# Kernel optimization log

Hardware: AMD Instinct MI355X
Metric: run time of the kernel (lower is better)

Reference implementation:

```python
import jax, jax.numpy as jnp
import numpy as np

HEADS = 16
D_MODEL = 1024
D_HEAD = D_MODEL // HEADS


def setup_inputs() -> dict:
    key = jax.random.key(0)
    ks = jax.random.split(key, 9)
    s_h = 1.0 / np.sqrt(D_HEAD)
    s_m = 1.0 / np.sqrt(D_MODEL)
    return {
        "x": jax.random.normal(ks[0], (4, 2048, D_MODEL), dtype=jnp.float32),
        "Wq": jax.random.uniform(ks[1], (D_HEAD, D_HEAD), jnp.float32, -s_h, s_h),
        "bq": jax.random.uniform(ks[2], (D_HEAD,), jnp.float32, -s_h, s_h),
        "Wk": jax.random.uniform(ks[3], (D_HEAD, D_HEAD), jnp.float32, -s_h, s_h),
        "bk": jax.random.uniform(ks[4], (D_HEAD,), jnp.float32, -s_h, s_h),
        "Wv": jax.random.uniform(ks[5], (D_HEAD, D_HEAD), jnp.float32, -s_h, s_h),
        "bv": jax.random.uniform(ks[6], (D_HEAD,), jnp.float32, -s_h, s_h),
        "Wp": jax.random.uniform(ks[7], (D_MODEL, D_MODEL), jnp.float32, -s_m, s_m),
        "bp": jax.random.uniform(ks[8], (D_MODEL,), jnp.float32, -s_m, s_m),
    }


def reference(x, Wq, bq, Wk, bk, Wv, bv, Wp, bp):
    B, T, C = x.shape
    xh = x.reshape(B, T, HEADS, D_HEAD)  # [B,T,H,Dh]
    # per-head linear projections (torch Linear: x @ W.T + b)
    q = jnp.einsum('bthd,ed->bhte', xh, Wq) + bq  # [B,H,T,Dh]
    k = jnp.einsum('bthd,ed->bhte', xh, Wk) + bk
    v = jnp.einsum('bthd,ed->bhte', xh, Wv) + bv
    # NOTE: original scales by sqrt(C) = sqrt(d_model), not sqrt(d_head)
    att = jnp.einsum('bhqd,bhkd->bhqk', q, k) / jnp.sqrt(jnp.float32(C))
    att = jax.nn.softmax(att, axis=-1)
    out = jnp.einsum('bhqk,bhkd->bhqd', att, v)  # [B,H,T,Dh]
    out = out.transpose(0, 2, 1, 3).reshape(B, T, C)
    return out @ Wp.T + bp
```

## Files before the change

### kernel.cpp

```cpp
#include <hip/hip_runtime.h>
#include <hip/hip_bf16.h>
#include <cstddef>

#define B_  4
#define T_  2048
#define H_  16
#define DH  64
#define C_  1024
#define BH  64

typedef float  f32x16 __attribute__((ext_vector_type(16)));
typedef __bf16 bf16x8 __attribute__((ext_vector_type(8)));
typedef __bf16 bf16x4 __attribute__((ext_vector_type(4)));

#define MFMA32(a, b, c) __builtin_amdgcn_mfma_f32_32x32x16_bf16(a, b, c, 0, 0, 0)


__device__ __forceinline__ unsigned cvt_pk_bf16(float lo, float hi) {
    unsigned r;
    asm("v_cvt_pk_bf16_f32 %0, %1, %2" : "=v"(r) : "v"(lo), "v"(hi));
    return r;
}

__global__ __launch_bounds__(256) void wconv_kernel(
    const float* __restrict__ Wq, const float* __restrict__ Wk,
    const float* __restrict__ Wv, __bf16* __restrict__ wqkv)
{
    const int tid = blockIdx.x * 256 + threadIdx.x;
    const float* srcs[3] = {Wq, Wk, Wv};
    const int mat = tid >> 10;
    const int off = (tid & 1023) * 4;
    const float4 w4 = *(const float4*)(srcs[mat] + off);
    const unsigned lo = ((unsigned)__builtin_bit_cast(unsigned short, (__bf16)w4.y) << 16)
                      | (unsigned)__builtin_bit_cast(unsigned short, (__bf16)w4.x);
    const unsigned hi = ((unsigned)__builtin_bit_cast(unsigned short, (__bf16)w4.w) << 16)
                      | (unsigned)__builtin_bit_cast(unsigned short, (__bf16)w4.z);
    uint2 p; p.x = lo; p.y = hi;
    *(uint2*)(wqkv + mat * 4096 + off) = p;
}

__global__ __launch_bounds__(256) void qkv_kernel(
    const float* __restrict__ x,
    const __bf16* __restrict__ wqkv,
    const float* __restrict__ bq, const float* __restrict__ bk,
    const float* __restrict__ bv,
    __bf16* __restrict__ q, __bf16* __restrict__ kf, __bf16* __restrict__ vf)
{
    __shared__ __bf16 Xs[128 * 72];
    __shared__ __bf16 Ws[3][64 * 72];
    __bf16* Vtl = Xs;
    __bf16* Kst = &Ws[0][0];

    const int tt  = blockIdx.x;
    const int bh  = blockIdx.y;
    const int b   = bh >> 4, h = bh & 15;
    const int t0  = tt * 128;
    const int tid = threadIdx.x;
    const int wave = tid >> 6, lane = tid & 63;
    const int m = lane & 31, hh = lane >> 5;

    #pragma unroll
    for (int i = 0; i < 8; ++i) {
        const int idx = i * 256 + tid;
        const int r = idx >> 4, c = (idx & 15) * 4;
        const float4 x4 = *(const float4*)(x + ((size_t)(b * T_ + t0 + r)) * C_ + h * DH + c);
        const unsigned lo = ((unsigned)__builtin_bit_cast(unsigned short, (__bf16)x4.y) << 16)
                          | (unsigned)__builtin_bit_cast(unsigned short, (__bf16)x4.x);
        const unsigned hi = ((unsigned)__builtin_bit_cast(unsigned short, (__bf16)x4.w) << 16)
                          | (unsigned)__builtin_bit_cast(unsigned short, (__bf16)x4.z);
        *(unsigned*)&Xs[r * 72 + c]     = lo;
        *(unsigned*)&Xs[r * 72 + c + 2] = hi;
    }
    #pragma unroll
    for (int i = 0; i < 6; ++i) {
        const int idx = i * 256 + tid;
        const int mat_ = idx >> 9;
        const int r = (idx >> 3) & 63, c = (idx & 7) * 8;
        *(uint4*)&Ws[mat_][r * 72 + c] = *(const uint4*)(wqkv + mat_ * 4096 + r * 64 + c);
    }
    __syncthreads();

    bf16x8 xf[4];
    #pragma unroll
    for (int ks = 0; ks < 4; ++ks)
        xf[ks] = *(const bf16x8*)&Xs[(wave * 32 + m) * 72 + ks * 16 + hh * 8];
    __syncthreads();

    const float s32 = 0.03125f * 1.4426950408889634f;

    unsigned kpk[16];

    #pragma unroll
    for (int mat = 0; mat < 3; ++mat) {
        f32x16 acc0 = {}, acc1 = {};
        #pragma unroll
        for (int ks = 0; ks < 4; ++ks) {
            const bf16x8 w0 = *(const bf16x8*)&Ws[mat][(m) * 72 + ks * 16 + hh * 8];
            const bf16x8 w1 = *(const bf16x8*)&Ws[mat][(32 + m) * 72 + ks * 16 + hh * 8];
            acc0 = MFMA32(xf[ks], w0, acc0);
            acc1 = MFMA32(xf[ks], w1, acc1);
        }
        const float* bias = (mat == 0) ? bq : (mat == 1) ? bk : bv;
        const float b0 = bias[m], b1 = bias[32 + m];
        #pragma unroll
        for (int r = 0; r < 16; ++r) {
            const int R = (r & 3) + 8 * (r >> 2) + 4 * hh;
            const int tloc = wave * 32 + R;
            const float v0 = acc0[r] + b0, v1 = acc1[r] + b1;
            if (mat == 0) {
                const size_t base = ((size_t)bh * T_ + t0 + tloc) * DH;
                q[base + m]      = (__bf16)(v0 * s32);
                q[base + 32 + m] = (__bf16)(v1 * s32);
            } else if (mat == 1) {
                kpk[r] = ((unsigned)__builtin_bit_cast(unsigned short, (__bf16)v1) << 16)
                       |  (unsigned)__builtin_bit_cast(unsigned short, (__bf16)v0);
            } else {
                Vtl[(m) * 136 + tloc]      = (__bf16)v0;
                Vtl[(32 + m) * 136 + tloc] = (__bf16)v1;
            }
        }
    }
    __syncthreads();

    #pragma unroll
    for (int r = 0; r < 16; ++r) {
        const int R = (r & 3) + 8 * (r >> 2) + 4 * hh;
        const int tloc = wave * 32 + R;
        Kst[tloc * 72 + m]      = __builtin_bit_cast(__bf16, (unsigned short)(kpk[r] & 0xffff));
        Kst[tloc * 72 + 32 + m] = __builtin_bit_cast(__bf16, (unsigned short)(kpk[r] >> 16));
    }

    #pragma unroll
    for (int i = 0; i < 4; ++i) {
        const int idx = i * 256 + tid;
        const int ln = idx & 63, c_ = idx >> 6;
        const int kt64l = c_ >> 3, dh = (c_ >> 2) & 1, cN = c_ & 3;
        const __bf16* src = &Vtl[(dh * 32 + (ln & 31)) * 136 + kt64l * 64 + cN * 16 + (ln >> 5) * 8];
        __bf16* dst = vf + ((((size_t)(bh * 32 + tt * 2 + kt64l) * 2 + dh) * 4 + cN) * 64 + ln) * 8;
        *(uint4*)dst = *(const uint4*)src;
    }
    __syncthreads();

    #pragma unroll
    for (int i = 0; i < 4; ++i) {
        const int idx = i * 256 + tid;
        const int ln = idx & 63, c_ = idx >> 6;
        const int kt64l = c_ >> 3, rh = (c_ >> 2) & 1, ks = c_ & 3;
        const __bf16* src = &Kst[(kt64l * 64 + rh * 32 + (ln & 31)) * 72 + ks * 16 + (ln >> 5) * 8];
        __bf16* dst = kf + ((((size_t)(bh * 32 + tt * 2 + kt64l) * 2 + rh) * 4 + ks) * 64 + ln) * 8;
        *(uint4*)dst = *(const uint4*)src;
    }
}

__global__ __launch_bounds__(256, 4) void attn_kernel(
    const __bf16* __restrict__ q, const __bf16* __restrict__ kf,
    const __bf16* __restrict__ vf, __bf16* __restrict__ o)
{
    __shared__ __bf16 Os[128 * 72];

    const int bh  = blockIdx.x;
    const int q0  = blockIdx.y * 128;
    const int tid = threadIdx.x;
    const int wave = tid >> 6, lane = tid & 63;
    const int m = lane & 31, h = lane >> 5;

    const __bf16* qb  = q  + (size_t)bh * T_ * DH;
    const __bf16* kfb = kf + (size_t)bh * (T_ * DH);
    const __bf16* vfb = vf + (size_t)bh * (T_ * DH);

    bf16x8 qf[4];
    #pragma unroll
    for (int ks = 0; ks < 4; ++ks)
        qf[ks] = *(const bf16x8*)(qb + (size_t)(q0 + wave * 32 + m) * DH + ks * 16 + h * 8);

    f32x16 O0 = {}, O1 = {};
    float lsum = 0.f;

    for (int kt = 0; kt < 32; ++kt) {
        const __bf16* kt_k = kfb + kt * 4096;
        const __bf16* kt_v = vfb + kt * 4096;
        #pragma unroll
        for (int rh = 0; rh < 2; ++rh) {
            bf16x8 kfr[4];
            #pragma unroll
            for (int ks = 0; ks < 4; ++ks)
                kfr[ks] = *(const bf16x8*)(kt_k + rh * 2048 + ks * 512 + lane * 8);
            f32x16 S = {};
            #pragma unroll
            for (int ks = 0; ks < 4; ++ks)
                S = MFMA32(kfr[ks], qf[ks], S);

            #pragma unroll
            for (int cc = 0; cc < 2; ++cc) {
                const int rb = cc * 8;
                float e0 = __builtin_amdgcn_exp2f(S[rb + 0]);
                float e1 = __builtin_amdgcn_exp2f(S[rb + 1]);
                float e2 = __builtin_amdgcn_exp2f(S[rb + 2]);
                float e3 = __builtin_amdgcn_exp2f(S[rb + 3]);
                float e4 = __builtin_amdgcn_exp2f(S[rb + 4]);
                float e5 = __builtin_amdgcn_exp2f(S[rb + 5]);
                float e6 = __builtin_amdgcn_exp2f(S[rb + 6]);
                float e7 = __builtin_amdgcn_exp2f(S[rb + 7]);
                lsum += ((e0 + e1) + (e2 + e3)) + ((e4 + e5) + (e6 + e7));
                unsigned a0 = cvt_pk_bf16(e0, e1);
                unsigned a1 = cvt_pk_bf16(e2, e3);
                unsigned b0 = cvt_pk_bf16(e4, e5);
                unsigned b1 = cvt_pk_bf16(e6, e7);
                asm("v_permlane32_swap_b32 %0, %1" : "+v"(a0), "+v"(b0));
                asm("v_permlane32_swap_b32 %0, %1" : "+v"(a1), "+v"(b1));
                const uint4 pw = {a0, a1, b0, b1};
                const bf16x8 pb = __builtin_bit_cast(bf16x8, pw);
                const int c = rh * 2 + cc;
                const bf16x8 v0 = *(const bf16x8*)(kt_v + c * 512 + lane * 8);
                const bf16x8 v1 = *(const bf16x8*)(kt_v + 2048 + c * 512 + lane * 8);
                O0 = MFMA32(v0, pb, O0);
                O1 = MFMA32(v1, pb, O1);
            }
        }
    }

    lsum += __shfl_xor(lsum, 32);
    const float linv = 1.0f / lsum;

    #pragma unroll
    for (int g = 0; g < 4; ++g) {
        bf16x4 w0, w1;
        #pragma unroll
        for (int j = 0; j < 4; ++j) {
            w0[j] = (__bf16)(O0[4 * g + j] * linv);
            w1[j] = (__bf16)(O1[4 * g + j] * linv);
        }
        const int row = (wave * 32 + m) * 72;
        *(bf16x4*)&Os[row + 8 * g + 4 * h]      = w0;
        *(bf16x4*)&Os[row + 32 + 8 * g + 4 * h] = w1;
    }
    __syncthreads();

    __bf16* ob = o + ((size_t)bh * T_ + q0) * DH;
    #pragma unroll
    for (int i = 0; i < 4; ++i) {
        const int idx = i * 256 + tid;
        const int r = idx >> 3, c = (idx & 7) * 8;
        *(uint4*)(ob + (size_t)r * DH + c) = *(uint4*)&Os[r * 72 + c];
    }
}

__global__ __launch_bounds__(256) void wpconv_kernel(
    const float* __restrict__ Wp, __bf16* __restrict__ Wpb)
{
    const size_t idx = (size_t)(blockIdx.x * 256 + threadIdx.x) * 4;
    const float4 w4 = *(const float4*)(Wp + idx);
    const unsigned lo = ((unsigned)__builtin_bit_cast(unsigned short, (__bf16)w4.y) << 16)
                      | (unsigned)__builtin_bit_cast(unsigned short, (__bf16)w4.x);
    const unsigned hi = ((unsigned)__builtin_bit_cast(unsigned short, (__bf16)w4.w) << 16)
                      | (unsigned)__builtin_bit_cast(unsigned short, (__bf16)w4.z);
    uint2 p; p.x = lo; p.y = hi;
    *(uint2*)(Wpb + idx) = p;
}

__global__ __launch_bounds__(256, 2) void proj_kernel(
    const __bf16* __restrict__ a,
    const __bf16* __restrict__ Wpb, const float* __restrict__ bp,
    float* __restrict__ out)
{
    __shared__ __bf16 As[2][128 * 72];
    __shared__ __bf16 Bs[2][128 * 72];

    const int tb = blockIdx.x, eb = blockIdx.y;
    const int tid = threadIdx.x;
    const int wave = tid >> 6, lane = tid & 63;
    const int m = lane & 31, h = lane >> 5;
    const int tok0 = tb * 128;
    const int b = tok0 >> 11, t0 = tok0 & (T_ - 1);
    const int e0 = eb * 128;

    auto aload = [&](int cb, uint4 (&ar)[4], uint4 (&br)[4]) {
        #pragma unroll
        for (int i = 0; i < 4; ++i) {
            const int idx = i * 256 + tid;
            const int r = idx >> 3, c = (idx & 7) * 8;
            ar[i] = *(const uint4*)(a + ((size_t)(b * H_ + cb) * T_ + t0 + r) * DH + c);
            br[i] = *(const uint4*)(Wpb + (size_t)(e0 + r) * C_ + cb * 64 + c);
        }
    };
    auto astore = [&](int buf, const uint4 (&ar)[4], const uint4 (&br)[4]) {
        #pragma unroll
        for (int i = 0; i < 4; ++i) {
            const int idx = i * 256 + tid;
            const int r = idx >> 3, c = (idx & 7) * 8;
            *(uint4*)&As[buf][r * 72 + c] = ar[i];
            *(uint4*)&Bs[buf][r * 72 + c] = br[i];
        }
    };

    f32x16 acc[4] = {f32x16{}, f32x16{}, f32x16{}, f32x16{}};
    uint4 areg[4], breg[4];

    aload(0, areg, breg);
    astore(0, areg, breg);

    int cur = 0;
    for (int cb = 0; cb < 16; ++cb) {
        __syncthreads();
        if (cb < 15) aload(cb + 1, areg, breg);

        #pragma unroll
        for (int ks = 0; ks < 4; ++ks) {
            const bf16x8 af = *(const bf16x8*)&As[cur][(wave * 32 + m) * 72 + ks * 16 + h * 8];
            #pragma unroll
            for (int n = 0; n < 4; ++n) {
                const bf16x8 bf = *(const bf16x8*)&Bs[cur][(n * 32 + m) * 72 + ks * 16 + h * 8];
                acc[n] = MFMA32(af, bf, acc[n]);
            }
        }

        if (cb < 15) astore(cur ^ 1, areg, breg);
        cur ^= 1;
    }

    #pragma unroll
    for (int n = 0; n < 4; ++n) {
        const int e = e0 + n * 32 + m;
        const float bias = bp[e];
        #pragma unroll
        for (int r = 0; r < 16; ++r) {
            const int R = (r & 3) + 8 * (r >> 2) + 4 * h;
            out[(size_t)(tok0 + wave * 32 + R) * C_ + e] = acc[n][r] + bias;
        }
    }
}

extern "C" void kernel_launch(void* const* d_in, const int* in_sizes, int n_in,
                              void* d_out, int out_size, void* d_ws, size_t ws_size,
                              hipStream_t stream)
{
    const float* x  = (const float*)d_in[0];
    const float* Wq = (const float*)d_in[1];
    const float* bq = (const float*)d_in[2];
    const float* Wk = (const float*)d_in[3];
    const float* bk = (const float*)d_in[4];
    const float* Wv = (const float*)d_in[5];
    const float* bv = (const float*)d_in[6];
    const float* Wp = (const float*)d_in[7];
    const float* bp = (const float*)d_in[8];

    const size_t N = (size_t)BH * T_ * DH;
    __bf16* qws  = (__bf16*)d_ws;
    __bf16* kws  = qws + N;
    __bf16* vtws = kws + N;
    __bf16* ows  = vtws + N;
    __bf16* wqkv = ows;
    __bf16* wpb  = qws;

    wconv_kernel<<<dim3(12), 256, 0, stream>>>(Wq, Wk, Wv, wqkv);
    qkv_kernel<<<dim3(16, 64), 256, 0, stream>>>(
        x, wqkv, bq, bk, bv, qws, kws, vtws);
    attn_kernel<<<dim3(64, 16), 256, 0, stream>>>(qws, kws, vtws, ows);
    wpconv_kernel<<<dim3(1024), 256, 0, stream>>>(Wp, wpb);
    proj_kernel<<<dim3(64, 8), 256, 0, stream>>>(ows, wpb, bp, (float*)d_out);
}
```

Measured before the change: 259.8 us.

## Store attention output and Wp in MFMA fragment order, drop LDS from proj

The attention kernel now writes its output in a pre-swizzled MFMA fragment layout, and the Wp conversion kernel emits bf16 weights in the same fragment order. This lets the projection GEMM load operands straight from global memory into registers with coalesced 16-byte loads, removing the LDS double buffering and barriers. The trade-off is that every block re-reads Wp fragments from global or L2 with no shared-memory reuse, and software prefetching is lost, so latency hiding depends on occupancy.

```diff
diff --git a/kernel.cpp b/kernel.cpp
--- a/kernel.cpp
+++ b/kernel.cpp
@@ -154,7 +154,7 @@
 
 __global__ __launch_bounds__(256, 4) void attn_kernel(
     const __bf16* __restrict__ q, const __bf16* __restrict__ kf,
-    const __bf16* __restrict__ vf, __bf16* __restrict__ o)
+    const __bf16* __restrict__ vf, __bf16* __restrict__ af)
 {
     __shared__ __bf16 Os[128 * 72];
 
@@ -236,86 +236,81 @@
     }
     __syncthreads();
 
-    __bf16* ob = o + ((size_t)bh * T_ + q0) * DH;
+    __bf16* ab = af + ((size_t)(bh * 16 + (q0 >> 7))) * 8192;
     #pragma unroll
     for (int i = 0; i < 4; ++i) {
         const int idx = i * 256 + tid;
-        const int r = idx >> 3, c = (idx & 7) * 8;
-        *(uint4*)(ob + (size_t)r * DH + c) = *(uint4*)&Os[r * 72 + c];
+        const int ln = idx & 63, c_ = idx >> 6;
+        const int wv = c_ >> 2, ks = c_ & 3;
+        const __bf16* src = &Os[(wv * 32 + (ln & 31)) * 72 + ks * 16 + (ln >> 5) * 8];
+        *(uint4*)(ab + c_ * 512 + ln * 8) = *(const uint4*)src;
     }
 }
 
 __global__ __launch_bounds__(256) void wpconv_kernel(
-    const float* __restrict__ Wp, __bf16* __restrict__ Wpb)
-{
-    const size_t idx = (size_t)(blockIdx.x * 256 + threadIdx.x) * 4;
-    const float4 w4 = *(const float4*)(Wp + idx);
-    const unsigned lo = ((unsigned)__builtin_bit_cast(unsigned short, (__bf16)w4.y) << 16)
-                      | (unsigned)__builtin_bit_cast(unsigned short, (__bf16)w4.x);
-    const unsigned hi = ((unsigned)__builtin_bit_cast(unsigned short, (__bf16)w4.w) << 16)
-                      | (unsigned)__builtin_bit_cast(unsigned short, (__bf16)w4.z);
-    uint2 p; p.x = lo; p.y = hi;
-    *(uint2*)(Wpb + idx) = p;
-}
-
-__global__ __launch_bounds__(256, 2) void proj_kernel(
-    const __bf16* __restrict__ a,
-    const __bf16* __restrict__ Wpb, const float* __restrict__ bp,
+    const float* __restrict__ Wp, __bf16* __restrict__ wpf)
+{
+    const int gtid = blockIdx.x * 256 + threadIdx.x;
+    #pragma unroll
+    for (int i = 0; i < 4; ++i) {
+        const int ci = gtid + i * 32768;
+        const int ln = ci & 63;
+        const int ks = (ci >> 6) & 3;
+        const int n  = (ci >> 8) & 3;
+        const int cb = (ci >> 10) & 15;
+        const int eb = ci >> 14;
+        const int row = eb * 128 + n * 32 + (ln & 31);
+        const int col = cb * 64 + ks * 16 + (ln >> 5) * 8;
+        const float4 w0 = *(const float4*)(Wp + (size_t)row * C_ + col);
+        const float4 w1 = *(const float4*)(Wp + (size_t)row * C_ + col + 4);
+        uint4 p;
+        p.x = ((unsigned)__builtin_bit_cast(unsigned short, (__bf16)w0.y) << 16)
+            |  (unsigned)__builtin_bit_cast(unsigned short, (__bf16)w0.x);
+        p.y = ((unsigned)__builtin_bit_cast(unsigned short, (__bf16)w0.w) << 16)
+            |  (unsigned)__builtin_bit_cast(unsigned short, (__bf16)w0.z);
+        p.z = ((unsigned)__builtin_bit_cast(unsigned short, (__bf16)w1.y) << 16)
+            |  (unsigned)__builtin_bit_cast(unsigned short, (__bf16)w1.x);
+        p.w = ((unsigned)__builtin_bit_cast(unsigned short, (__bf16)w1.w) << 16)
+            |  (unsigned)__builtin_bit_cast(unsigned short, (__bf16)w1.z);
+        *(uint4*)(wpf + (size_t)ci * 8) = p;
+    }
+}
+
+__global__ __launch_bounds__(256) void proj_kernel(
+    const __bf16* __restrict__ af,
+    const __bf16* __restrict__ wpf,
+    const float* __restrict__ bp,
     float* __restrict__ out)
 {
-    __shared__ __bf16 As[2][128 * 72];
-    __shared__ __bf16 Bs[2][128 * 72];
-
     const int tb = blockIdx.x, eb = blockIdx.y;
     const int tid = threadIdx.x;
     const int wave = tid >> 6, lane = tid & 63;
     const int m = lane & 31, h = lane >> 5;
     const int tok0 = tb * 128;
-    const int b = tok0 >> 11, t0 = tok0 & (T_ - 1);
+    const int b = tb >> 4, qtile = tb & 15;
     const int e0 = eb * 128;
 
-    auto aload = [&](int cb, uint4 (&ar)[4], uint4 (&br)[4]) {
-        #pragma unroll
-        for (int i = 0; i < 4; ++i) {
-            const int idx = i * 256 + tid;
-            const int r = idx >> 3, c = (idx & 7) * 8;
-            ar[i] = *(const uint4*)(a + ((size_t)(b * H_ + cb) * T_ + t0 + r) * DH + c);
-            br[i] = *(const uint4*)(Wpb + (size_t)(e0 + r) * C_ + cb * 64 + c);
-        }
-    };
-    auto astore = [&](int buf, const uint4 (&ar)[4], const uint4 (&br)[4]) {
-        #pragma unroll
-        for (int i = 0; i < 4; ++i) {
-            const int idx = i * 256 + tid;
-            const int r = idx >> 3, c = (idx & 7) * 8;
-            *(uint4*)&As[buf][r * 72 + c] = ar[i];
-            *(uint4*)&Bs[buf][r * 72 + c] = br[i];
-        }
-    };
+    const __bf16* abase = af + ((size_t)(b * 256 + qtile)) * 8192
+                             + (wave * 4) * 512 + lane * 8;
+    const __bf16* wbase = wpf + (size_t)eb * 131072 + lane * 8;
 
     f32x16 acc[4] = {f32x16{}, f32x16{}, f32x16{}, f32x16{}};
-    uint4 areg[4], breg[4];
-
-    aload(0, areg, breg);
-    astore(0, areg, breg);
-
-    int cur = 0;
+
     for (int cb = 0; cb < 16; ++cb) {
-        __syncthreads();
-        if (cb < 15) aload(cb + 1, areg, breg);
-
-        #pragma unroll
-        for (int ks = 0; ks < 4; ++ks) {
-            const bf16x8 af = *(const bf16x8*)&As[cur][(wave * 32 + m) * 72 + ks * 16 + h * 8];
+        const __bf16* ap = abase + (size_t)cb * 131072;
+        const __bf16* wp = wbase + (size_t)cb * 8192;
+        bf16x8 afr[4];
+        #pragma unroll
+        for (int ks = 0; ks < 4; ++ks)
+            afr[ks] = *(const bf16x8*)(ap + ks * 512);
+        #pragma unroll
+        for (int n = 0; n < 4; ++n) {
             #pragma unroll
-            for (int n = 0; n < 4; ++n) {
-                const bf16x8 bf = *(const bf16x8*)&Bs[cur][(n * 32 + m) * 72 + ks * 16 + h * 8];
-                acc[n] = MFMA32(af, bf, acc[n]);
+            for (int ks = 0; ks < 4; ++ks) {
+                const bf16x8 bf = *(const bf16x8*)(wp + (n * 4 + ks) * 512);
+                acc[n] = MFMA32(afr[ks], bf, acc[n]);
             }
         }
-
-        if (cb < 15) astore(cur ^ 1, areg, breg);
-        cur ^= 1;
     }
 
     #pragma unroll
@@ -348,14 +343,14 @@
     __bf16* qws  = (__bf16*)d_ws;
     __bf16* kws  = qws + N;
     __bf16* vtws = kws + N;
-    __bf16* ows  = vtws + N;
-    __bf16* wqkv = ows;
-    __bf16* wpb  = qws;
+    __bf16* aws  = vtws + N;
+    __bf16* wqkv = aws;
+    __bf16* wpf  = qws;
 
     wconv_kernel<<<dim3(12), 256, 0, stream>>>(Wq, Wk, Wv, wqkv);
     qkv_kernel<<<dim3(16, 64), 256, 0, stream>>>(
         x, wqkv, bq, bk, bv, qws, kws, vtws);
-    attn_kernel<<<dim3(64, 16), 256, 0, stream>>>(qws, kws, vtws, ows);
-    wpconv_kernel<<<dim3(1024), 256, 0, stream>>>(Wp, wpb);
-    proj_kernel<<<dim3(64, 8), 256, 0, stream>>>(ows, wpb, bp, (float*)d_out);
-}
+    attn_kernel<<<dim3(64, 16), 256, 0, stream>>>(qws, kws, vtws, aws);
+    wpconv_kernel<<<dim3(128), 256, 0, stream>>>(Wp, wpf);
+    proj_kernel<<<dim3(64, 8), 256, 0, stream>>>(aws, wpf, bp, (float*)d_out);
+}
```

After: 248.7 us. -4.3%, faster.
